# Kernel tuning notes

Hardware: AMD Instinct MI355X
Metric: run time of the kernel (lower is better)

Reference implementation:

```python
import jax, jax.numpy as jnp
import numpy as np

B, N, C, H, P = 8, 4096, 512, 8, 64
D = C // H


def setup_inputs() -> dict:
    key = jax.random.key(0)
    ks = jax.random.split(key, 5)
    s = 0.02
    return {
        "x": jax.random.normal(ks[0], (B, N, C), jnp.float32),
        "w_qkv": jax.random.normal(ks[1], (3 * C, C), jnp.float32) * s,
        "w_e": jax.random.normal(ks[2], (P, N), jnp.float32) * s,
        "b_e": jnp.zeros((P,), jnp.float32),
        "temperature": jnp.ones((1, 1, 1), jnp.float32),
        "temperature2": jnp.ones((H, 1, 1), jnp.float32),
        "w_o1": jax.random.normal(ks[3], (C // 2, C), jnp.float32) * s,
        "b_o1": jnp.zeros((C // 2,), jnp.float32),
        "w_o2": jax.random.normal(ks[4], (C // 2, C), jnp.float32) * s,
        "b_o2": jnp.zeros((C // 2,), jnp.float32),
    }


def reference(x, w_qkv, w_e, b_e, temperature, temperature2, w_o1, b_o1, w_o2, b_o2):
    Bs, Ns, Cs = x.shape
    # qkvv projection and head split: [B,N,3C] -> [3,B,H,N,D]
    qkv = (x @ w_qkv.T).reshape(Bs, Ns, 3, H, D)
    qkv = jnp.transpose(qkv, (2, 0, 3, 1, 4))
    q, k, v = qkv[0], qkv[1], qkv[2]
    q_t = jnp.swapaxes(q, -2, -1)  # [B,H,D,N]
    k_t = jnp.swapaxes(k, -2, -1)  # [B,H,D,N]
    v_t = jnp.swapaxes(v, -2, -1)  # [B,H,D,N]
    # Linformer-style projection along token axis; E = F (shared weights)
    kp = k_t @ w_e.T + b_e  # [B,H,D,P]
    vp = v_t @ w_e.T + b_e  # [B,H,D,P]
    # L2-normalize q along tokens (k is normalized in the original AFTER
    # projection, so that normalization is dead code and omitted)
    qn = q_t / jnp.maximum(jnp.linalg.norm(q_t, axis=-1, keepdims=True), 1e-12)
    # ---- channel attention: [B,C,C] scores over raw x ----
    xt = jnp.swapaxes(x, -2, -1)  # [B,C,N]
    attn_ca = jax.nn.softmax((xt @ x) * temperature, axis=-1)
    x_ca = jnp.swapaxes(attn_ca @ xt, -2, -1)  # [B,N,C]
    # ---- projected spatial attention: [B,H,N,P] scores ----
    attn_sa = jax.nn.softmax(
        jnp.einsum('bhdn,bhdp->bhnp', qn, kp) * temperature2, axis=-1)
    x_sa = jnp.einsum('bhnp,bhdp->bhnd', attn_sa, vp)  # [B,H,N,D]
    # faithful to torch: permute(0,3,1,2) then reshape(B,N,C)
    x_sa = jnp.transpose(x_sa, (0, 3, 1, 2)).reshape(Bs, Ns, Cs)
    out = jnp.concatenate(
        [x_sa @ w_o1.T + b_o1, x_ca @ w_o2.T + b_o2], axis=-1)
    return out
```

## Files before the change

### kernel.cpp

```cpp
#include <hip/hip_runtime.h>
#include <hip/hip_bf16.h>

typedef unsigned short u16;

#define AS1 __attribute__((address_space(1)))
#define AS3 __attribute__((address_space(3)))

static __device__ __forceinline__ float bl(u16 v) {
    return __uint_as_float(((unsigned)v) << 16);
}
static __device__ __forceinline__ u16 f2b(float f) {
    unsigned u = __float_as_uint(f);
    unsigned r = u + 0x7FFFu + ((u >> 16) & 1u);
    return (u16)(r >> 16);
}
static __device__ __forceinline__ float ldf(const void* p, long i, int isbf) {
    if (isbf) return bl(((const u16*)p)[i]);
    return ((const float*)p)[i];
}
static __device__ __forceinline__ void gload_lds16(const u16* g, u16* l) {
    __builtin_amdgcn_global_load_lds((const AS1 void*)g, (AS3 void*)l, 16, 0, 0);
}

typedef __attribute__((ext_vector_type(8))) short bf16x8;
typedef __attribute__((ext_vector_type(4))) float f32x4;

static __device__ __forceinline__ bf16x8 pack8(const float* p) {
    const float4 x0 = ((const float4*)p)[0];
    const float4 x1 = ((const float4*)p)[1];
    unsigned r0, r1, r2, r3;
    asm("v_cvt_pk_bf16_f32 %0, %1, %2" : "=v"(r0) : "v"(x0.x), "v"(x0.y));
    asm("v_cvt_pk_bf16_f32 %0, %1, %2" : "=v"(r1) : "v"(x0.z), "v"(x0.w));
    asm("v_cvt_pk_bf16_f32 %0, %1, %2" : "=v"(r2) : "v"(x1.x), "v"(x1.y));
    asm("v_cvt_pk_bf16_f32 %0, %1, %2" : "=v"(r3) : "v"(x1.z), "v"(x1.w));
    union { unsigned u[4]; bf16x8 v; } u;
    u.u[0] = r0; u.u[1] = r1; u.u[2] = r2; u.u[3] = r3;
    return u.v;
}

__global__ void dtype_probe(const void* __restrict__ temp, unsigned* __restrict__ flag) {
    if (threadIdx.x == 0 && blockIdx.x == 0)
        flag[0] = (((const u16*)temp)[0] == 0x3F80) ? 1u : 0u;
}

__global__ __launch_bounds__(256) void zero_f32(float* __restrict__ p, long n) {
    const long stride = (long)gridDim.x * 256;
    for (long i = (long)blockIdx.x * 256 + threadIdx.x; i < n; i += stride)
        p[i] = 0.f;
}

__global__ __launch_bounds__(256) void conv_x(const void* __restrict__ X,
                                              u16* __restrict__ xb,
                                              u16* __restrict__ xt,
                                              const unsigned* __restrict__ flg)
{
    __shared__ u16 tile[64][65];
    const int f = (int)flg[0];
    const int b = blockIdx.z;
    const int n0 = blockIdx.x * 64, c0 = blockIdx.y * 64;
    const int t = threadIdx.x, r0 = t >> 6, c = t & 63;
    #pragma unroll
    for (int rr = 0; rr < 16; ++rr) {
        const int r = rr * 4 + r0;
        const long gi = ((long)b * 4096 + n0 + r) * 512 + c0 + c;
        const u16 h = f2b(ldf(X, gi, f));
        xb[gi] = h;
        tile[r][c] = h;
    }
    __syncthreads();
    #pragma unroll
    for (int rr = 0; rr < 16; ++rr) {
        const int cc = rr * 4 + r0;
        xt[((long)b * 512 + c0 + cc) * 4096 + n0 + c] = tile[c][cc];
    }
}

__global__ __launch_bounds__(256) void conv_w(const void* __restrict__ W,
                                              u16* __restrict__ wb, long nelem,
                                              const unsigned* __restrict__ flg)
{
    const int f = (int)flg[0];
    const long stride = (long)gridDim.x * 256;
    for (long i = (long)blockIdx.x * 256 + threadIdx.x; i < nelem; i += stride)
        wb[i] = f2b(ldf(W, i, f));
}

__global__ __launch_bounds__(512, 2) void gemm256_nt(
    const u16* __restrict__ A, const u16* __restrict__ B,
    void* __restrict__ C, const void* __restrict__ bias,
    int K, int lda, int ldb, int ldc,
    long sA, long sB, long sC,
    const unsigned* __restrict__ flg, int biasExt, int cF32,
    float* __restrict__ qsq,
    const u16* __restrict__ A2, const u16* __restrict__ B2,
    const void* __restrict__ bias2, int nSwitch)
{
    __shared__ u16 Asm[2][256 * 32];
    __shared__ u16 Bsm[2][256 * 32];
    const int t = threadIdx.x, w = t >> 6, l = t & 63;
    const int gx = gridDim.x, gy = gridDim.y;
    const long nwg = (long)gx * gy * gridDim.z;
    const long lin = blockIdx.x + (long)gx * (blockIdx.y + (long)gy * blockIdx.z);
    long nid = lin;
    if ((nwg & 7) == 0) nid = (lin & 7) * (nwg >> 3) + (lin >> 3);
    const int by = (int)(nid % gy);
    const long r2 = nid / gy;
    const int bx = (int)(r2 % gx);
    const int bz = (int)(r2 / gx);
    const int m0 = bx * 256, n0 = by * 256;
    const u16* Asel = A; const u16* Bsel = B; const void* bsel = bias;
    int nLoc = n0;
    if (A2 && n0 >= nSwitch) { Asel = A2; Bsel = B2; bsel = bias2; nLoc = n0 - nSwitch; }
    const u16* Ab = Asel + (long)bz * sA;
    const u16* Bb = Bsel + (long)bz * sB + (long)nLoc * ldb;
    const int wm = (w >> 1) * 64, wn = (w & 1) * 128;
    const int srow = l >> 2;
    const int selem = (((l & 3) ^ (srow & 3)) << 3);
    const int fr = l & 15;
    const int fk = (l >> 4) * 8;
    const int xorv = (fr & 3) << 3;
    f32x4 acc[4][8];
    #pragma unroll
    for (int i = 0; i < 4; ++i)
        #pragma unroll
        for (int j = 0; j < 8; ++j)
            acc[i][j] = (f32x4){0.f, 0.f, 0.f, 0.f};

#define STAGE256(nb, kk)                                                                     \
    do {                                                                                     \
        gload_lds16(Ab + (long)(m0 + w * 16 + srow) * lda + (kk) + selem, &Asm[nb][w * 512]);        \
        gload_lds16(Ab + (long)(m0 + (w + 8) * 16 + srow) * lda + (kk) + selem, &Asm[nb][(w + 8) * 512]); \
        gload_lds16(Bb + (long)(w * 16 + srow) * ldb + (kk) + selem, &Bsm[nb][w * 512]);             \
        gload_lds16(Bb + (long)((w + 8) * 16 + srow) * ldb + (kk) + selem, &Bsm[nb][(w + 8) * 512]);     \
    } while (0)

    STAGE256(0, 0);
    __syncthreads();
    int cur = 0;
    for (int k0 = 0; k0 < K; k0 += 32) {
        if (k0 + 32 < K) STAGE256(cur ^ 1, k0 + 32);
        bf16x8 af[4], bf[8];
        #pragma unroll
        for (int i = 0; i < 4; ++i)
            af[i] = *(const bf16x8*)&Asm[cur][((wm + i * 16 + fr) << 5) + (fk ^ xorv)];
        #pragma unroll
        for (int j = 0; j < 8; ++j)
            bf[j] = *(const bf16x8*)&Bsm[cur][((wn + j * 16 + fr) << 5) + (fk ^ xorv)];
        #pragma unroll
        for (int i = 0; i < 4; ++i)
            #pragma unroll
            for (int j = 0; j < 8; ++j)
                acc[i][j] = __builtin_amdgcn_mfma_f32_16x16x32_bf16(af[i], bf[j], acc[i][j], 0, 0, 0);
        __syncthreads();
        cur ^= 1;
    }
#undef STAGE256

    const int f = (int)flg[0];
    const long cOff = (long)bz * sC;
    float bj[8];
    #pragma unroll
    for (int j = 0; j < 8; ++j) bj[j] = 0.f;
    if (bsel) {
        #pragma unroll
        for (int j = 0; j < 8; ++j)
            bj[j] = ldf(bsel, (nLoc & 255) + wn + j * 16 + fr, biasExt ? f : 1);
    }
    #pragma unroll
    for (int i = 0; i < 4; ++i) {
        #pragma unroll
        for (int j = 0; j < 8; ++j) {
            const int col = n0 + wn + j * 16 + fr;
            #pragma unroll
            for (int r = 0; r < 4; ++r) {
                const int row = m0 + wm + i * 16 + (l >> 4) * 4 + r;
                const float v = acc[i][j][r] + bj[j];
                if (cF32) ((float*)C)[cOff + (long)row * ldc + col] = v;
                else      ((u16*)C)[cOff + (long)row * ldc + col] = f2b(v);
            }
        }
    }
    if (qsq) {
        #pragma unroll
        for (int j = 0; j < 8; ++j) {
            const int col = n0 + wn + j * 16 + fr;
            if (col < 512) {
                float s = 0.f;
                #pragma unroll
                for (int i = 0; i < 4; ++i)
                    #pragma unroll
                    for (int r = 0; r < 4; ++r)
                        s = fmaf(acc[i][j][r], acc[i][j][r], s);
                s += __shfl_xor(s, 16, 64);
                s += __shfl_xor(s, 32, 64);
                if ((l >> 4) == 0)
                    atomicAdd(&qsq[(long)bz * 512 + col], s);
            }
        }
    }
}

__global__ __launch_bounds__(256) void gram128_sym(
    const u16* __restrict__ XT, float* __restrict__ SP)
{
    __shared__ u16 Asm[2][128 * 32];
    __shared__ u16 Bsm[2][128 * 32];
    const int t = threadIdx.x, w = t >> 6, l = t & 63;
    const int tx = blockIdx.x, b = blockIdx.y, kz = blockIdx.z;
    int ti, tj;
    if (tx < 4)      { ti = 0; tj = tx; }
    else if (tx < 7) { ti = 1; tj = tx - 3; }
    else if (tx < 9) { ti = 2; tj = tx - 5; }
    else             { ti = 3; tj = 3; }
    const int diag = (ti == tj);
    const int m0 = ti * 128, n0 = tj * 128;
    const u16* Ab = XT + (long)b * 512 * 4096 + (long)m0 * 4096;
    const u16* Bb = XT + (long)b * 512 * 4096 + (long)n0 * 4096;
    const int wm = (w >> 1) * 64, wn = (w & 1) * 64;
    const int srow = l >> 2;
    const int scol = (l & 3) * 8;
    const int fr = l & 15;
    const int fk = (l >> 4) * 8;
    f32x4 acc[4][4];
    #pragma unroll
    for (int i = 0; i < 4; ++i)
        #pragma unroll
        for (int j = 0; j < 4; ++j)
            acc[i][j] = (f32x4){0.f, 0.f, 0.f, 0.f};

    const int q0 = w, q1 = w + 4;
#define GSTAGE(nb, kk)                                                                  \
    do {                                                                                \
        gload_lds16(Ab + (long)(q0 * 16 + srow) * 4096 + (kk) + scol, &Asm[nb][q0 * 512]);      \
        gload_lds16(Ab + (long)(q1 * 16 + srow) * 4096 + (kk) + scol, &Asm[nb][q1 * 512]);      \
        if (!diag) {                                                                    \
            gload_lds16(Bb + (long)(q0 * 16 + srow) * 4096 + (kk) + scol, &Bsm[nb][q0 * 512]);  \
            gload_lds16(Bb + (long)(q1 * 16 + srow) * 4096 + (kk) + scol, &Bsm[nb][q1 * 512]);  \
        }                                                                               \
    } while (0)

    const int kBeg = kz * 1024, kEnd = kBeg + 1024;
    GSTAGE(0, kBeg);
    __syncthreads();
    int cur = 0;
    for (int k0 = kBeg; k0 < kEnd; k0 += 32) {
        if (k0 + 32 < kEnd) GSTAGE(cur ^ 1, k0 + 32);
        const u16* Bsrc = diag ? &Asm[cur][0] : &Bsm[cur][0];
        bf16x8 af[4], bf[4];
        #pragma unroll
        for (int i = 0; i < 4; ++i) {
            af[i] = *(const bf16x8*)&Asm[cur][(wm + i * 16 + fr) * 32 + fk];
            bf[i] = *(const bf16x8*)&Bsrc[(wn + i * 16 + fr) * 32 + fk];
        }
        #pragma unroll
        for (int i = 0; i < 4; ++i)
            #pragma unroll
            for (int j = 0; j < 4; ++j)
                acc[i][j] = __builtin_amdgcn_mfma_f32_16x16x32_bf16(af[i], bf[j], acc[i][j], 0, 0, 0);
        __syncthreads();
        cur ^= 1;
    }
#undef GSTAGE

    float* Sb = SP + ((long)kz * 8 + b) * 262144;
    #pragma unroll
    for (int i = 0; i < 4; ++i) {
        #pragma unroll
        for (int j = 0; j < 4; ++j) {
            const int col = n0 + wn + j * 16 + fr;
            #pragma unroll
            for (int r = 0; r < 4; ++r) {
                const int row = m0 + wm + i * 16 + (l >> 4) * 4 + r;
                const float v = acc[i][j][r];
                Sb[(long)row * 512 + col] = v;
                if (!diag) Sb[(long)col * 512 + row] = v;
            }
        }
    }
}

__global__ __launch_bounds__(256) void xe_mfma(const u16* __restrict__ WEB,
                                               const u16* __restrict__ XT,
                                               float* __restrict__ XE)
{
    const int t = threadIdx.x, w = t >> 6, l = t & 63;
    const int l15 = l & 15, g = l >> 4;
    const int c0 = blockIdx.x * 128 + (w >> 1) * 64;
    const int b = blockIdx.y;
    const int nbase = blockIdx.z * 512 + (w & 1) * 256;
    f32x4 acc[4][4];
    #pragma unroll
    for (int i = 0; i < 4; ++i)
        #pragma unroll
        for (int j = 0; j < 4; ++j)
            acc[i][j] = (f32x4){0.f, 0.f, 0.f, 0.f};
    for (int ks = 0; ks < 8; ++ks) {
        const int n = nbase + ks * 32 + g * 8;
        bf16x8 a[4], bb[4];
        #pragma unroll
        for (int i = 0; i < 4; ++i)
            a[i] = *(const bf16x8*)&WEB[(long)(i * 16 + l15) * 4096 + n];
        #pragma unroll
        for (int j = 0; j < 4; ++j)
            bb[j] = *(const bf16x8*)&XT[((long)b * 512 + c0 + j * 16 + l15) * 4096 + n];
        #pragma unroll
        for (int i = 0; i < 4; ++i)
            #pragma unroll
            for (int j = 0; j < 4; ++j)
                acc[i][j] = __builtin_amdgcn_mfma_f32_16x16x32_bf16(a[i], bb[j], acc[i][j], 0, 0, 0);
    }
    #pragma unroll
    for (int i = 0; i < 4; ++i)
        #pragma unroll
        for (int j = 0; j < 4; ++j)
            #pragma unroll
            for (int r = 0; r < 4; ++r)
                atomicAdd(&XE[((long)b * 64 + i * 16 + g * 4 + r) * 512 + c0 + j * 16 + l15],
                          acc[i][j][r]);
}

__global__ __launch_bounds__(256) void kpvp2_mfma(const float* __restrict__ XE,
                                                  const u16* __restrict__ WQB,
                                                  const float* __restrict__ qsq,
                                                  const void* __restrict__ be,
                                                  const void* __restrict__ temp2,
                                                  u16* __restrict__ kpT,
                                                  u16* __restrict__ vpB,
                                                  const unsigned* __restrict__ flg)
{
    __shared__ float lds[4][4096];
    const int bh = blockIdx.x, b = bh >> 3, h = bh & 7;
    const int t = threadIdx.x, w = t >> 6, l = t & 63;
    const int l15 = l & 15, g = l >> 4;
    const int isV = w >> 1;
    const int ch = w & 1;
    const u16* wrow = WQB + (long)(512 + isV * 512 + h * 64) * 512;
    const float* xr = XE + (long)b * 64 * 512;
    f32x4 acc[4][4];
    #pragma unroll
    for (int i = 0; i < 4; ++i)
        #pragma unroll
        for (int j = 0; j < 4; ++j)
            acc[i][j] = (f32x4){0.f, 0.f, 0.f, 0.f};
    for (int ks = 0; ks < 8; ++ks) {
        const int c = ch * 256 + ks * 32 + g * 8;
        bf16x8 a[4], bb[4];
        if (!isV) {
            #pragma unroll
            for (int i = 0; i < 4; ++i)
                a[i] = pack8(&xr[(long)(i * 16 + l15) * 512 + c]);
            #pragma unroll
            for (int j = 0; j < 4; ++j)
                bb[j] = *(const bf16x8*)&wrow[(long)(j * 16 + l15) * 512 + c];
        } else {
            #pragma unroll
            for (int i = 0; i < 4; ++i)
                a[i] = *(const bf16x8*)&wrow[(long)(i * 16 + l15) * 512 + c];
            #pragma unroll
            for (int j = 0; j < 4; ++j)
                bb[j] = pack8(&xr[(long)(j * 16 + l15) * 512 + c]);
        }
        #pragma unroll
        for (int i = 0; i < 4; ++i)
            #pragma unroll
            for (int j = 0; j < 4; ++j)
                acc[i][j] = __builtin_amdgcn_mfma_f32_16x16x32_bf16(a[i], bb[j], acc[i][j], 0, 0, 0);
    }
    #pragma unroll
    for (int i = 0; i < 4; ++i)
        #pragma unroll
        for (int j = 0; j < 4; ++j)
            #pragma unroll
            for (int r = 0; r < 4; ++r)
                lds[w][(i * 16 + g * 4 + r) * 64 + j * 16 + l15] = acc[i][j][r];
    __syncthreads();
    const int f = (int)flg[0];
    if (t < 128) {
        const float t2 = ldf(temp2, h, f);
        for (int e = t; e < 4096; e += 128) {
            const int p = e >> 6, d = e & 63;
            const float rn = 1.0f / fmaxf(sqrtf(qsq[b * 512 + h * 64 + d]), 1e-12f);
            kpT[(long)bh * 4096 + e] = f2b((lds[0][e] + lds[1][e] + ldf(be, p, f)) * rn * t2);
        }
    } else {
        for (int e = t - 128; e < 4096; e += 128) {
            vpB[(long)bh * 4096 + e] = f2b(lds[2][e] + lds[3][e] + ldf(be, e & 63, f));
        }
    }
}

__global__ __launch_bounds__(256) void softmax_ca(const float* __restrict__ SP,
                                                  u16* __restrict__ A,
                                                  const void* __restrict__ temp,
                                                  const unsigned* __restrict__ flg)
{
    __shared__ float red[256];
    const int row = blockIdx.x;
    const int t = threadIdx.x;
    const float tv = ldf(temp, 0, (int)flg[0]);
    const float* s = SP + (long)row * 512;
    const long kzs = (long)8 * 512 * 512;
    float v0 = s[t] + s[kzs + t] + s[2 * kzs + t] + s[3 * kzs + t];
    float v1 = s[t + 256] + s[kzs + t + 256] + s[2 * kzs + t + 256] + s[3 * kzs + t + 256];
    v0 *= tv;
    v1 *= tv;
    red[t] = fmaxf(v0, v1);
    __syncthreads();
    for (int o = 128; o > 0; o >>= 1) {
        if (t < o) red[t] = fmaxf(red[t], red[t + o]);
        __syncthreads();
    }
    const float m = red[0];
    __syncthreads();
    float e0 = expf(v0 - m), e1 = expf(v1 - m);
    red[t] = e0 + e1;
    __syncthreads();
    for (int o = 128; o > 0; o >>= 1) {
        if (t < o) red[t] += red[t + o];
        __syncthreads();
    }
    const float inv = 1.0f / red[0];
    u16* a = A + (long)row * 512;
    a[t]       = f2b(e0 * inv);
    a[t + 256] = f2b(e1 * inv);
}

__global__ __launch_bounds__(256) void spatial_attn_mfma(
    const u16* __restrict__ Q, const u16* __restrict__ kpT,
    const u16* __restrict__ vpB, u16* __restrict__ XSA)
{
    __shared__ u16 P[4][4096];
    const int bh = blockIdx.y, b = bh >> 3, h = bh & 7;
    const int t = threadIdx.x, w = t >> 6, l = t & 63;
    const int l15 = l & 15, g = l >> 4;
    const int n0 = blockIdx.x * 256 + w * 64;
    char* Pw = (char*)&P[w][0];

    const u16* kb = kpT + (long)bh * 4096;
    const u16* vb = vpB + (long)bh * 4096;
    bf16x8 akp[2][4], avp[2][4];
    #pragma unroll
    for (int ks = 0; ks < 2; ++ks)
        #pragma unroll
        for (int i = 0; i < 4; ++i) {
            akp[ks][i] = *(const bf16x8*)&kb[(i * 16 + l15) * 64 + ks * 32 + g * 8];
            avp[ks][i] = *(const bf16x8*)&vb[(i * 16 + l15) * 64 + ks * 32 + g * 8];
        }

    f32x4 sacc[4][4];
    #pragma unroll
    for (int i = 0; i < 4; ++i)
        #pragma unroll
        for (int j = 0; j < 4; ++j)
            sacc[i][j] = (f32x4){0.f, 0.f, 0.f, 0.f};
    const u16* qb = Q + ((long)b * 4096 + n0) * 512 + h * 64;
    #pragma unroll
    for (int ks = 0; ks < 2; ++ks) {
        bf16x8 bq[4];
        #pragma unroll
        for (int j = 0; j < 4; ++j)
            bq[j] = *(const bf16x8*)&qb[(long)(j * 16 + l15) * 512 + ks * 32 + g * 8];
        #pragma unroll
        for (int i = 0; i < 4; ++i)
            #pragma unroll
            for (int j = 0; j < 4; ++j)
                sacc[i][j] = __builtin_amdgcn_mfma_f32_16x16x32_bf16(akp[ks][i], bq[j], sacc[i][j], 0, 0, 0);
    }

    #pragma unroll
    for (int j = 0; j < 4; ++j) {
        float m = sacc[0][j][0];
        #pragma unroll
        for (int i = 0; i < 4; ++i)
            #pragma unroll
            for (int r = 0; r < 4; ++r)
                m = fmaxf(m, sacc[i][j][r]);
        m = fmaxf(m, __shfl_xor(m, 16, 64));
        m = fmaxf(m, __shfl_xor(m, 32, 64));
        float s = 0.f;
        #pragma unroll
        for (int i = 0; i < 4; ++i)
            #pragma unroll
            for (int r = 0; r < 4; ++r) {
                const float e = __expf(sacc[i][j][r] - m);
                sacc[i][j][r] = e;
                s += e;
            }
        s += __shfl_xor(s, 16, 64);
        s += __shfl_xor(s, 32, 64);
        const float inv = 1.0f / s;
        const int n = j * 16 + l15;
        const int swz = (n & 7) << 4;
        #pragma unroll
        for (int i = 0; i < 4; ++i) {
            unsigned lo, hi;
            float p0 = sacc[i][j][0] * inv, p1 = sacc[i][j][1] * inv;
            float p2 = sacc[i][j][2] * inv, p3 = sacc[i][j][3] * inv;
            asm("v_cvt_pk_bf16_f32 %0, %1, %2" : "=v"(lo) : "v"(p0), "v"(p1));
            asm("v_cvt_pk_bf16_f32 %0, %1, %2" : "=v"(hi) : "v"(p2), "v"(p3));
            const int byte = (n * 128 + i * 32 + g * 8) ^ swz;
            *(uint2*)(Pw + byte) = make_uint2(lo, hi);
        }
    }

    f32x4 oacc[4][4];
    #pragma unroll
    for (int i = 0; i < 4; ++i)
        #pragma unroll
        for (int j = 0; j < 4; ++j)
            oacc[i][j] = (f32x4){0.f, 0.f, 0.f, 0.f};
    #pragma unroll
    for (int ks = 0; ks < 2; ++ks) {
        bf16x8 bp[4];
        #pragma unroll
        for (int j = 0; j < 4; ++j) {
            const int n = j * 16 + l15;
            const int byte = (n * 128 + ks * 64 + g * 16) ^ ((n & 7) << 4);
            bp[j] = *(const bf16x8*)(Pw + byte);
        }
        #pragma unroll
        for (int i = 0; i < 4; ++i)
            #pragma unroll
            for (int j = 0; j < 4; ++j)
                oacc[i][j] = __builtin_amdgcn_mfma_f32_16x16x32_bf16(avp[ks][i], bp[j], oacc[i][j], 0, 0, 0);
    }

    const int rowoff = h * 8 + (n0 >> 9);
    const int colbase = n0 & 511;
    #pragma unroll
    for (int i = 0; i < 4; ++i)
        #pragma unroll
        for (int r = 0; r < 4; ++r) {
            const int d = i * 16 + g * 4 + r;
            u16* orow = XSA + ((long)b * 4096 + d * 64 + rowoff) * 512 + colbase;
            #pragma unroll
            for (int j = 0; j < 4; ++j)
                orow[j * 16 + l15] = f2b(oacc[i][j][r]);
        }
}

extern "C" void kernel_launch(void* const* d_in, const int* in_sizes, int n_in,
                              void* d_out, int out_size, void* d_ws, size_t ws_size,
                              hipStream_t stream)
{
    const void* x     = d_in[0];
    const void* w_qkv = d_in[1];
    const void* w_e   = d_in[2];
    const void* b_e   = d_in[3];
    const void* temp  = d_in[4];
    const void* temp2 = d_in[5];
    const void* w_o1  = d_in[6];
    const void* b_o1  = d_in[7];
    const void* w_o2  = d_in[8];
    const void* b_o2  = d_in[9];
    float* out = (float*)d_out;

    char* ws = (char*)d_ws;
    unsigned* flag = (unsigned*)ws; ws += 256;
    u16*   qb     = (u16*)ws;   ws += (size_t)8 * 4096 * 512 * 2;
    float* qsq    = (float*)ws; ws += (size_t)4096 * 4;
    float* xe     = (float*)ws; ws += (size_t)8 * 64 * 512 * 4;
    float* scpart = (float*)ws; ws += (size_t)4 * 8 * 512 * 512 * 4;
    u16*   attn   = (u16*)ws;   ws += (size_t)8 * 512 * 512 * 2;
    u16*   x_ca   = (u16*)ws;   ws += (size_t)8 * 4096 * 512 * 2;
    u16*   xt     = (u16*)ws;   ws += (size_t)8 * 512 * 4096 * 2;
    u16*   xb     = (u16*)ws;   ws += (size_t)8 * 4096 * 512 * 2;
    u16*   wqb    = (u16*)ws;   ws += (size_t)1536 * 512 * 2;
    u16*   web    = (u16*)ws;   ws += (size_t)64 * 4096 * 2;
    u16*   wo1b   = (u16*)ws;   ws += (size_t)256 * 512 * 2;
    u16*   wo2b   = (u16*)ws;   ws += (size_t)256 * 512 * 2;
    u16*   kpT    = (u16*)ws;   ws += (size_t)262144 * 2;
    u16*   vpB    = (u16*)ws;   ws += (size_t)262144 * 2;
    u16*   x_sa   = xt;

    dtype_probe<<<1, 64, 0, stream>>>(temp, flag);
    conv_x<<<dim3(64, 8, 8), 256, 0, stream>>>(x, xb, xt, flag);
    conv_w<<<768, 256, 0, stream>>>(w_qkv, wqb, 1536L * 512, flag);
    conv_w<<<128, 256, 0, stream>>>(w_e, web, 64L * 4096, flag);
    conv_w<<<128, 256, 0, stream>>>(w_o1, wo1b, 256L * 512, flag);
    conv_w<<<128, 256, 0, stream>>>(w_o2, wo2b, 256L * 512, flag);
    zero_f32<<<4, 256, 0, stream>>>(qsq, 4096);
    gemm256_nt<<<dim3(16, 2, 8), 512, 0, stream>>>(
        xb, wqb, qb, nullptr, 512, 512, 512, 512,
        (long)4096 * 512, 0, (long)4096 * 512, flag, 0, 0, qsq,
        nullptr, nullptr, nullptr, 1 << 30);
    zero_f32<<<128, 256, 0, stream>>>(xe, (long)8 * 64 * 512);
    xe_mfma<<<dim3(4, 8, 8), 256, 0, stream>>>(web, xt, xe);
    kpvp2_mfma<<<64, 256, 0, stream>>>(xe, wqb, qsq, b_e, temp2, kpT, vpB, flag);
    gram128_sym<<<dim3(10, 8, 4), 256, 0, stream>>>(xt, scpart);
    softmax_ca<<<4096, 256, 0, stream>>>(scpart, attn, temp, flag);
    gemm256_nt<<<dim3(16, 2, 8), 512, 0, stream>>>(
        xb, attn, x_ca, nullptr, 512, 512, 512, 512,
        (long)4096 * 512, (long)512 * 512, (long)4096 * 512, flag, 0, 0, nullptr,
        nullptr, nullptr, nullptr, 1 << 30);
    spatial_attn_mfma<<<dim3(16, 64), 256, 0, stream>>>(qb, kpT, vpB, x_sa);
    gemm256_nt<<<dim3(16, 2, 8), 512, 0, stream>>>(
        x_sa, wo1b, out, b_o1, 512, 512, 512, 512,
        (long)4096 * 512, 0, (long)4096 * 512, flag, 1, 1, nullptr,
        x_ca, wo2b, b_o2, 256);
}
```

Baseline: 374.4 us.

## Fold channel-attention output projection into attention matrix via reassociation

Instead of computing x_ca = x·attnᵀ (a full B×N×C GEMM) and then projecting it by w_o2, the code precomputes M2 = w_o2·attn per batch (a small 256×512 GEMM) and feeds x with M2 directly into the final output GEMM. This drops one large GEMM and the x_ca intermediate write and read. Separately, the Gram split-K is doubled from 4 to 8 chunks to raise parallelism, which makes the softmax read more partial sums. The reassociation changes the rounding order, since M2 is stored in bf16.

```diff
diff --git a/kernel.cpp b/kernel.cpp
--- a/kernel.cpp
+++ b/kernel.cpp
@@ -93,7 +93,7 @@
     const unsigned* __restrict__ flg, int biasExt, int cF32,
     float* __restrict__ qsq,
     const u16* __restrict__ A2, const u16* __restrict__ B2,
-    const void* __restrict__ bias2, int nSwitch)
+    const void* __restrict__ bias2, int nSwitch, long sB2)
 {
     __shared__ u16 Asm[2][256 * 32];
     __shared__ u16 Bsm[2][256 * 32];
@@ -109,10 +109,11 @@
     const int bz = (int)(r2 / gx);
     const int m0 = bx * 256, n0 = by * 256;
     const u16* Asel = A; const u16* Bsel = B; const void* bsel = bias;
+    long sBv = sB;
     int nLoc = n0;
-    if (A2 && n0 >= nSwitch) { Asel = A2; Bsel = B2; bsel = bias2; nLoc = n0 - nSwitch; }
+    if (A2 && n0 >= nSwitch) { Asel = A2; Bsel = B2; bsel = bias2; nLoc = n0 - nSwitch; sBv = sB2; }
     const u16* Ab = Asel + (long)bz * sA;
-    const u16* Bb = Bsel + (long)bz * sB + (long)nLoc * ldb;
+    const u16* Bb = Bsel + (long)bz * sBv + (long)nLoc * ldb;
     const int wm = (w >> 1) * 64, wn = (w & 1) * 128;
     const int srow = l >> 2;
     const int selem = (((l & 3) ^ (srow & 3)) << 3);
@@ -239,7 +240,7 @@
         }                                                                               \
     } while (0)
 
-    const int kBeg = kz * 1024, kEnd = kBeg + 1024;
+    const int kBeg = kz * 512, kEnd = kBeg + 512;
     GSTAGE(0, kBeg);
     __syncthreads();
     int cur = 0;
@@ -274,6 +275,68 @@
                 const float v = acc[i][j][r];
                 Sb[(long)row * 512 + col] = v;
                 if (!diag) Sb[(long)col * 512 + row] = v;
+            }
+        }
+    }
+}
+
+__global__ __launch_bounds__(256) void m2_gemm(const u16* __restrict__ WO2,
+                                               const u16* __restrict__ ATTN,
+                                               u16* __restrict__ M2)
+{
+    __shared__ u16 Asm[128 * 32];
+    __shared__ u16 Bsm[128 * 48];
+    const int t = threadIdx.x, w = t >> 6, l = t & 63;
+    const int m0 = blockIdx.x * 128, n0 = blockIdx.y * 128, b = blockIdx.z;
+    const u16* At = ATTN + (long)b * 262144;
+    const int wm = (w >> 1) * 64, wn = (w & 1) * 64;
+    const int srow = l >> 2, scol = (l & 3) * 8;
+    const int fr = l & 15, fk = (l >> 4) * 8;
+    const int br = t >> 3;
+    const int bc = (t & 7) * 16;
+    f32x4 acc[4][4];
+    #pragma unroll
+    for (int i = 0; i < 4; ++i)
+        #pragma unroll
+        for (int j = 0; j < 4; ++j)
+            acc[i][j] = (f32x4){0.f, 0.f, 0.f, 0.f};
+
+    for (int k0 = 0; k0 < 512; k0 += 32) {
+        __syncthreads();
+        gload_lds16(WO2 + (long)(m0 + w * 16 + srow) * 512 + k0 + scol, &Asm[w * 512]);
+        gload_lds16(WO2 + (long)(m0 + (w + 4) * 16 + srow) * 512 + k0 + scol, &Asm[(w + 4) * 512]);
+        {
+            const u16* src = At + (long)(k0 + br) * 512 + n0 + bc;
+            u16 tmp[16];
+            #pragma unroll
+            for (int i = 0; i < 16; ++i) tmp[i] = src[i];
+            #pragma unroll
+            for (int i = 0; i < 16; ++i) Bsm[(bc + i) * 48 + br] = tmp[i];
+        }
+        __syncthreads();
+        bf16x8 af[4], bf[4];
+        #pragma unroll
+        for (int i = 0; i < 4; ++i) {
+            af[i] = *(const bf16x8*)&Asm[(wm + i * 16 + fr) * 32 + fk];
+            bf[i] = *(const bf16x8*)&Bsm[(wn + i * 16 + fr) * 48 + fk];
+        }
+        #pragma unroll
+        for (int i = 0; i < 4; ++i)
+            #pragma unroll
+            for (int j = 0; j < 4; ++j)
+                acc[i][j] = __builtin_amdgcn_mfma_f32_16x16x32_bf16(af[i], bf[j], acc[i][j], 0, 0, 0);
+    }
+
+    u16* Mb = M2 + (long)b * 131072;
+    #pragma unroll
+    for (int i = 0; i < 4; ++i) {
+        #pragma unroll
+        for (int j = 0; j < 4; ++j) {
+            const int col = n0 + wn + j * 16 + fr;
+            #pragma unroll
+            for (int r = 0; r < 4; ++r) {
+                const int row = m0 + wm + i * 16 + (l >> 4) * 4 + r;
+                Mb[(long)row * 512 + col] = f2b(acc[i][j][r]);
             }
         }
     }
@@ -400,8 +463,12 @@
     const float tv = ldf(temp, 0, (int)flg[0]);
     const float* s = SP + (long)row * 512;
     const long kzs = (long)8 * 512 * 512;
-    float v0 = s[t] + s[kzs + t] + s[2 * kzs + t] + s[3 * kzs + t];
-    float v1 = s[t + 256] + s[kzs + t + 256] + s[2 * kzs + t + 256] + s[3 * kzs + t + 256];
+    float v0 = 0.f, v1 = 0.f;
+    #pragma unroll
+    for (int z = 0; z < 8; ++z) {
+        v0 += s[z * kzs + t];
+        v1 += s[z * kzs + t + 256];
+    }
     v0 *= tv;
     v1 *= tv;
     red[t] = fmaxf(v0, v1);
@@ -560,9 +627,9 @@
     u16*   qb     = (u16*)ws;   ws += (size_t)8 * 4096 * 512 * 2;
     float* qsq    = (float*)ws; ws += (size_t)4096 * 4;
     float* xe     = (float*)ws; ws += (size_t)8 * 64 * 512 * 4;
-    float* scpart = (float*)ws; ws += (size_t)4 * 8 * 512 * 512 * 4;
+    float* scpart = (float*)ws; ws += (size_t)8 * 8 * 512 * 512 * 4;
     u16*   attn   = (u16*)ws;   ws += (size_t)8 * 512 * 512 * 2;
-    u16*   x_ca   = (u16*)ws;   ws += (size_t)8 * 4096 * 512 * 2;
+    u16*   m2     = (u16*)ws;   ws += (size_t)8 * 256 * 512 * 2;
     u16*   xt     = (u16*)ws;   ws += (size_t)8 * 512 * 4096 * 2;
     u16*   xb     = (u16*)ws;   ws += (size_t)8 * 4096 * 512 * 2;
     u16*   wqb    = (u16*)ws;   ws += (size_t)1536 * 512 * 2;
@@ -583,19 +650,16 @@
     gemm256_nt<<<dim3(16, 2, 8), 512, 0, stream>>>(
         xb, wqb, qb, nullptr, 512, 512, 512, 512,
         (long)4096 * 512, 0, (long)4096 * 512, flag, 0, 0, qsq,
-        nullptr, nullptr, nullptr, 1 << 30);
+        nullptr, nullptr, nullptr, 1 << 30, 0);
     zero_f32<<<128, 256, 0, stream>>>(xe, (long)8 * 64 * 512);
     xe_mfma<<<dim3(4, 8, 8), 256, 0, stream>>>(web, xt, xe);
     kpvp2_mfma<<<64, 256, 0, stream>>>(xe, wqb, qsq, b_e, temp2, kpT, vpB, flag);
-    gram128_sym<<<dim3(10, 8, 4), 256, 0, stream>>>(xt, scpart);
+    gram128_sym<<<dim3(10, 8, 8), 256, 0, stream>>>(xt, scpart);
     softmax_ca<<<4096, 256, 0, stream>>>(scpart, attn, temp, flag);
-    gemm256_nt<<<dim3(16, 2, 8), 512, 0, stream>>>(
-        xb, attn, x_ca, nullptr, 512, 512, 512, 512,
-        (long)4096 * 512, (long)512 * 512, (long)4096 * 512, flag, 0, 0, nullptr,
-        nullptr, nullptr, nullptr, 1 << 30);
+    m2_gemm<<<dim3(2, 4, 8), 256, 0, stream>>>(wo2b, attn, m2);
     spatial_attn_mfma<<<dim3(16, 64), 256, 0, stream>>>(qb, kpT, vpB, x_sa);
     gemm256_nt<<<dim3(16, 2, 8), 512, 0, stream>>>(
         x_sa, wo1b, out, b_o1, 512, 512, 512, 512,
         (long)4096 * 512, 0, (long)4096 * 512, flag, 1, 1, nullptr,
-        x_ca, wo2b, b_o2, 256);
-}
+        xb, m2, b_o2, 256, (long)256 * 512);
+}
```

New measurement: 374.2 us. Within noise of the previous version (-0.1%).
